# Kernel optimization log

Hardware: AMD Instinct MI355X
Metric: run time of the kernel (lower is better)

Reference implementation:

```python
import jax, jax.numpy as jnp
import numpy as np

S, B, C = 7, 2, 4
N = 5 * B + C
LAMBDA_BOX = LAMBDA_CLS = LAMBDA_DF = 1.0
BATCH = 16384


def setup_inputs() -> dict:
    key = jax.random.key(0)
    k1, k2, k3 = jax.random.split(key, 3)
    shape = (BATCH, S, S, N)
    pred = jax.random.uniform(k1, shape, jnp.float32, 0.02, 0.98)
    target = jax.random.uniform(k2, shape, jnp.float32, 0.02, 0.98)
    obj = (jax.random.uniform(k3, (BATCH, S, S)) < 0.3).astype(jnp.float32)
    # confidence channels of both target bboxes carry the 0/1 object indicator
    target = target.at[..., 4].set(obj).at[..., 9].set(obj)
    return {"pred_tensor": pred, "target_tensor": target}


def _bce(p, t):
    # elementwise binary cross entropy (sum applied by caller)
    return -(t * jnp.log(p) + (1.0 - t) * jnp.log(1.0 - p))


def reference(pred_tensor, target_tensor):
    conf_t = target_tensor[..., 4]                       # [b,S,S]
    coord = (conf_t > 0).astype(pred_tensor.dtype)       # object cells

    pb = pred_tensor[..., :5 * B].reshape(*pred_tensor.shape[:-1], B, 5)   # [b,S,S,B,5]
    tb = target_tensor[..., :5 * B].reshape(*target_tensor.shape[:-1], B, 5)

    # xywh (cell coords) -> xyxy (image coords), as in the torch loop
    p_xy = pb[..., :2] / S
    p_wh = pb[..., 2:4]
    p_lt = p_xy - 0.5 * p_wh
    p_rb = p_xy + 0.5 * p_wh
    t0 = tb[..., 0, :]                                   # first target box of the group
    t_xy = t0[..., :2] / S
    t_wh = t0[..., 2:4]
    t_lt = t_xy - 0.5 * t_wh
    t_rb = t_xy + 0.5 * t_wh

    lt = jnp.maximum(p_lt, t_lt[..., None, :])
    rb = jnp.minimum(p_rb, t_rb[..., None, :])
    wh = jnp.clip(rb - lt, 0.0)
    inter = wh[..., 0] * wh[..., 1]                      # [b,S,S,B]
    area_p = (p_rb[..., 0] - p_lt[..., 0]) * (p_rb[..., 1] - p_lt[..., 1])
    area_t = ((t_rb[..., 0] - t_lt[..., 0]) * (t_rb[..., 1] - t_lt[..., 1]))[..., None]
    iou = inter / (area_p + area_t - inter)              # [b,S,S,B]

    max_iou = jnp.max(iou, axis=-1)                      # [b,S,S]
    idx = jnp.argmax(iou, axis=-1)                       # responsible bbox index
    resp_p = jnp.take_along_axis(pb, idx[..., None, None], axis=-2)[..., 0, :]  # [b,S,S,5]
    resp_t = jnp.take_along_axis(tb, idx[..., None, None], axis=-2)[..., 0, :]

    loss_xy = jnp.sum(coord * jnp.sum((resp_p[..., :2] - resp_t[..., :2]) ** 2, -1))
    loss_wh = jnp.sum(coord * jnp.sum((jnp.sqrt(resp_p[..., 2:4]) - jnp.sqrt(resp_t[..., 2:4])) ** 2, -1))
    loss_obj = jnp.sum(coord * (resp_p[..., 4] - max_iou) ** 2)

    loss_cls = jnp.sum(coord[..., None] * _bce(pred_tensor[..., 5 * B:], target_tensor[..., 5 * B:]))

    # focal-style df term over ALL cells (the original triple loop)
    q = conf_t
    p = pred_tensor[..., 4]
    alpha = (1.0 - q) / (1.0 - p)
    loss_df = jnp.sum(alpha * (p - q) * jnp.log(p) + (q - p) * jnp.log(1.0 - p))

    total = LAMBDA_BOX * (loss_xy + loss_wh + loss_obj) + LAMBDA_CLS * loss_cls + LAMBDA_DF * loss_df
    return total
```

## Files before the change

kernel.cpp:

```cpp
#include <hip/hip_runtime.h>


#define NPAIRS (16384 * 7 * 7 / 2)
#define TPB 64
#define PPW 64
#define PPB (2 * PPW)
#define SLOTS (PPW * 7)
#define NBLOCKS (NPAIRS / PPB)

typedef __attribute__((address_space(3))) void lds_void;
typedef const __attribute__((address_space(1))) void glb_void;

__device__ __forceinline__ float cell_loss(const float* __restrict__ p,
                                           const float* __restrict__ t) {
    const float conf_t = t[4];
    const float coord = (conf_t > 0.0f) ? 1.0f : 0.0f;

    const float tx = t[0] / 7.0f;
    const float ty = t[1] / 7.0f;
    const float tw = t[2];
    const float th = t[3];
    const float tlx = tx - 0.5f * tw, tly = ty - 0.5f * th;
    const float trx = tx + 0.5f * tw, trY = ty + 0.5f * th;
    const float area_t = (trx - tlx) * (trY - tly);

    float iou0, iou1;
    {
        const float px = p[0] / 7.0f, py = p[1] / 7.0f;
        const float pw = p[2], ph = p[3];
        const float plx = px - 0.5f * pw, ply = py - 0.5f * ph;
        const float prx = px + 0.5f * pw, prY = py + 0.5f * ph;
        const float ltx = fmaxf(plx, tlx), lty = fmaxf(ply, tly);
        const float rbx = fminf(prx, trx), rby = fminf(prY, trY);
        const float wx = fmaxf(rbx - ltx, 0.0f), wy = fmaxf(rby - lty, 0.0f);
        const float inter = wx * wy;
        const float area_p = (prx - plx) * (prY - ply);
        iou0 = inter / (area_p + area_t - inter);
    }
    {
        const float px = p[5] / 7.0f, py = p[6] / 7.0f;
        const float pw = p[7], ph = p[8];
        const float plx = px - 0.5f * pw, ply = py - 0.5f * ph;
        const float prx = px + 0.5f * pw, prY = py + 0.5f * ph;
        const float ltx = fmaxf(plx, tlx), lty = fmaxf(ply, tly);
        const float rbx = fminf(prx, trx), rby = fminf(prY, trY);
        const float wx = fmaxf(rbx - ltx, 0.0f), wy = fmaxf(rby - lty, 0.0f);
        const float inter = wx * wy;
        const float area_p = (prx - plx) * (prY - ply);
        iou1 = inter / (area_p + area_t - inter);
    }

    const bool sel1 = (iou1 > iou0);
    const float max_iou = fmaxf(iou0, iou1);

    const float rp0 = sel1 ? p[5] : p[0];
    const float rp1 = sel1 ? p[6] : p[1];
    const float rp2 = sel1 ? p[7] : p[2];
    const float rp3 = sel1 ? p[8] : p[3];
    const float rp4 = sel1 ? p[9] : p[4];
    const float rt0 = sel1 ? t[5] : t[0];
    const float rt1 = sel1 ? t[6] : t[1];
    const float rt2 = sel1 ? t[7] : t[2];
    const float rt3 = sel1 ? t[8] : t[3];

    const float dx = rp0 - rt0;
    const float dy = rp1 - rt1;
    const float l_xy = dx * dx + dy * dy;

    const float sw = sqrtf(rp2) - sqrtf(rt2);
    const float sh = sqrtf(rp3) - sqrtf(rt3);
    const float l_wh = sw * sw + sh * sh;

    const float dobj = rp4 - max_iou;
    const float l_obj = dobj * dobj;

    float l_cls = 0.0f;
#pragma unroll
    for (int c = 10; c < 14; ++c) {
        const float pc = p[c];
        const float tc = t[c];
        l_cls += -(tc * logf(pc) + (1.0f - tc) * logf(1.0f - pc));
    }

    const float q = conf_t;
    const float pp = p[4];
    const float alpha = (1.0f - q) / (1.0f - pp);
    const float l_df = alpha * (pp - q) * logf(pp) + (q - pp) * logf(1.0f - pp);

    return coord * (l_xy + l_wh + l_obj + l_cls) + l_df;
}

__global__ __launch_bounds__(TPB) void yolo_loss_kernel(
    const float* __restrict__ pred, const float* __restrict__ tgt,
    float* __restrict__ partials) {
    __shared__ float4 sp[2][SLOTS];
    __shared__ float4 st[2][SLOTS];

    const int lane = threadIdx.x;

    const long base4 = (long)blockIdx.x * (2 * SLOTS);
    const float4* __restrict__ gp = reinterpret_cast<const float4*>(pred) + base4;
    const float4* __restrict__ gt = reinterpret_cast<const float4*>(tgt) + base4;

#pragma unroll
    for (int h = 0; h < 2; ++h) {
#pragma unroll
        for (int it = 0; it < 7; ++it) {
            const int s = h * SLOTS + it * 64;
            const int d = it * 64;
            __builtin_amdgcn_global_load_lds((glb_void*)(gp + s + lane),
                                             (lds_void*)(&sp[h][d]), 16, 0, 0);
            __builtin_amdgcn_global_load_lds((glb_void*)(gt + s + lane),
                                             (lds_void*)(&st[h][d]), 16, 0, 0);
        }
    }

    float v = 0.0f;

    asm volatile("s_waitcnt vmcnt(14)" ::: "memory");
    {
        float lp[28], lt[28];
#pragma unroll
        for (int j = 0; j < 7; ++j) {
            const int s = 7 * lane + j;
            reinterpret_cast<float4*>(lp)[j] = sp[0][s];
            reinterpret_cast<float4*>(lt)[j] = st[0][s];
        }
        v += cell_loss(lp, lt) + cell_loss(lp + 14, lt + 14);
    }

    asm volatile("s_waitcnt vmcnt(0)" ::: "memory");
    {
        float lp[28], lt[28];
#pragma unroll
        for (int j = 0; j < 7; ++j) {
            const int s = 7 * lane + j;
            reinterpret_cast<float4*>(lp)[j] = sp[1][s];
            reinterpret_cast<float4*>(lt)[j] = st[1][s];
        }
        v += cell_loss(lp, lt) + cell_loss(lp + 14, lt + 14);
    }

#pragma unroll
    for (int off = 32; off > 0; off >>= 1) v += __shfl_down(v, off, 64);
    if (lane == 0) partials[blockIdx.x] = v;
}

__global__ __launch_bounds__(1024) void reduce_kernel(
    const float4* __restrict__ partials4, float* __restrict__ out) {
    const int tid = threadIdx.x;
    float v = 0.0f;
    if (tid < NBLOCKS / 4) {
        const float4 x = partials4[tid];
        v = (x.x + x.y) + (x.z + x.w);
    }
#pragma unroll
    for (int off = 32; off > 0; off >>= 1) v += __shfl_down(v, off, 64);
    __shared__ float s[16];
    if ((tid & 63) == 0) s[tid >> 6] = v;
    __syncthreads();
    if (tid == 0) {
        float r = 0.0f;
#pragma unroll
        for (int i = 0; i < 16; ++i) r += s[i];
        out[0] = r;
    }
}

extern "C" void kernel_launch(void* const* d_in, const int* in_sizes, int n_in,
                              void* d_out, int out_size, void* d_ws, size_t ws_size,
                              hipStream_t stream) {
    const float* pred = (const float*)d_in[0];
    const float* tgt  = (const float*)d_in[1];
    float* out = (float*)d_out;
    float* partials = (float*)d_ws;

    yolo_loss_kernel<<<NBLOCKS, TPB, 0, stream>>>(pred, tgt, partials);
    reduce_kernel<<<1, 1024, 0, stream>>>(
        reinterpret_cast<const float4*>(partials), out);
}
```

Measured before the change: 110.3 us.

## Process four tiles per block with a double-buffered LDS load ring

Each single-wave block now handles four 64-pair tiles instead of two. It streams them through two LDS buffers, issuing the next tile's global-to-LDS loads right after copying the current buffer to registers. This halves the block count and is meant to overlap memory loads with the loss math while amortizing per-block overhead. In exchange there are fewer waves resident, so fewer total bytes may be in flight, and correctness depends on hand-placed vmcnt/lgkmcnt waits.

```diff
diff --git a/kernel.cpp b/kernel.cpp
--- a/kernel.cpp
+++ b/kernel.cpp
@@ -4,9 +4,9 @@
 #define NPAIRS (16384 * 7 * 7 / 2)
 #define TPB 64
 #define PPW 64
-#define PPB (2 * PPW)
-#define SLOTS (PPW * 7)
-#define NBLOCKS (NPAIRS / PPB)
+#define NT 4
+#define TSLOTS (PPW * 7)
+#define NBLOCKS (NPAIRS / (PPW * NT))
 
 typedef __attribute__((address_space(3))) void lds_void;
 typedef const __attribute__((address_space(1))) void glb_void;
@@ -93,53 +93,57 @@
 __global__ __launch_bounds__(TPB) void yolo_loss_kernel(
     const float* __restrict__ pred, const float* __restrict__ tgt,
     float* __restrict__ partials) {
-    __shared__ float4 sp[2][SLOTS];
-    __shared__ float4 st[2][SLOTS];
+    __shared__ float4 sp[2][TSLOTS];
+    __shared__ float4 st[2][TSLOTS];
 
     const int lane = threadIdx.x;
 
-    const long base4 = (long)blockIdx.x * (2 * SLOTS);
+    const long base4 = (long)blockIdx.x * (NT * TSLOTS);
     const float4* __restrict__ gp = reinterpret_cast<const float4*>(pred) + base4;
     const float4* __restrict__ gt = reinterpret_cast<const float4*>(tgt) + base4;
 
-#pragma unroll
-    for (int h = 0; h < 2; ++h) {
-#pragma unroll
-        for (int it = 0; it < 7; ++it) {
-            const int s = h * SLOTS + it * 64;
-            const int d = it * 64;
-            __builtin_amdgcn_global_load_lds((glb_void*)(gp + s + lane),
-                                             (lds_void*)(&sp[h][d]), 16, 0, 0);
-            __builtin_amdgcn_global_load_lds((glb_void*)(gt + s + lane),
-                                             (lds_void*)(&st[h][d]), 16, 0, 0);
-        }
+#define ISSUE_TILE(buf, tile)                                                 \
+    {                                                                         \
+        _Pragma("unroll") for (int it = 0; it < 7; ++it) {                    \
+            const int gs = (tile) * TSLOTS + it * 64;                         \
+            const int ds = it * 64;                                           \
+            __builtin_amdgcn_global_load_lds((glb_void*)(gp + gs + lane),     \
+                                             (lds_void*)(&sp[buf][ds]), 16,   \
+                                             0, 0);                           \
+            __builtin_amdgcn_global_load_lds((glb_void*)(gt + gs + lane),     \
+                                             (lds_void*)(&st[buf][ds]), 16,   \
+                                             0, 0);                           \
+        }                                                                     \
     }
+
+    ISSUE_TILE(0, 0)
+    ISSUE_TILE(1, 1)
 
     float v = 0.0f;
 
-    asm volatile("s_waitcnt vmcnt(14)" ::: "memory");
-    {
+#pragma unroll
+    for (int i = 0; i < NT; ++i) {
+        const int buf = i & 1;
+        if (i < NT - 1) {
+            asm volatile("s_waitcnt vmcnt(14)" ::: "memory");
+        } else {
+            asm volatile("s_waitcnt vmcnt(0)" ::: "memory");
+        }
+
         float lp[28], lt[28];
 #pragma unroll
         for (int j = 0; j < 7; ++j) {
             const int s = 7 * lane + j;
-            reinterpret_cast<float4*>(lp)[j] = sp[0][s];
-            reinterpret_cast<float4*>(lt)[j] = st[0][s];
+            reinterpret_cast<float4*>(lp)[j] = sp[buf][s];
+            reinterpret_cast<float4*>(lt)[j] = st[buf][s];
         }
+        asm volatile("s_waitcnt lgkmcnt(0)" ::: "memory");
+
+        if (i + 2 < NT) ISSUE_TILE(buf, i + 2)
+
         v += cell_loss(lp, lt) + cell_loss(lp + 14, lt + 14);
     }
-
-    asm volatile("s_waitcnt vmcnt(0)" ::: "memory");
-    {
-        float lp[28], lt[28];
-#pragma unroll
-        for (int j = 0; j < 7; ++j) {
-            const int s = 7 * lane + j;
-            reinterpret_cast<float4*>(lp)[j] = sp[1][s];
-            reinterpret_cast<float4*>(lt)[j] = st[1][s];
-        }
-        v += cell_loss(lp, lt) + cell_loss(lp + 14, lt + 14);
-    }
+#undef ISSUE_TILE
 
 #pragma unroll
     for (int off = 32; off > 0; off >>= 1) v += __shfl_down(v, off, 64);
```

New measurement: 114.2 us. 1.04x slower.
